# Kernel tuning notes

Measured on AMD Instinct MI355X. Metric: run time of the kernel, lower is better.

Reference implementation:

```python
import jax, jax.numpy as jnp
import numpy as np

B, S, H = 1, 4096, 2048
NH, NKV, HD = 8, 4, 256
I = 8192
EPS = 1e-6
THETA = 10000.0
WINDOW = 4096  # hardcoded sliding window for even layer_idx
LAYER_IDX = 0


def rms_norm(x, w):
    v = jnp.mean(jnp.square(x), axis=-1, keepdims=True)
    return x * jax.lax.rsqrt(v + EPS) * w


def rotate_half(x):
    h = x.shape[-1] // 2
    return jnp.concatenate([-x[..., h:], x[..., :h]], axis=-1)


def apply_rope(q, k, positions):
    # q: [B,S,NH,HD], k: [B,S,NKV,HD], positions: [B,S]
    inv_freq = 1.0 / (THETA ** (jnp.arange(0, HD, 2, dtype=jnp.float32) / HD))
    freqs = positions.astype(jnp.float32)[..., None] * inv_freq  # [B,S,HD/2]
    emb = jnp.concatenate([freqs, freqs], axis=-1)               # [B,S,HD]
    cos = jnp.cos(emb)[:, :, None, :]
    sin = jnp.sin(emb)[:, :, None, :]
    q = q * cos + rotate_half(q) * sin
    k = k * cos + rotate_half(k) * sin
    return q, k


def forward(hidden_states, q_w, k_w, v_w, o_w, gate_w, up_w, down_w, ln1_w, ln2_w,
            attention_mask, position_ids):
    # ---- input RMSNorm + attention ----
    residual = hidden_states
    x = rms_norm(hidden_states, ln1_w)

    q = (x @ q_w).reshape(B, S, NH, HD)
    k = (x @ k_w).reshape(B, S, NKV, HD)
    v = (x @ v_w).reshape(B, S, NKV, HD)
    q, k = apply_rope(q, k, position_ids)

    # GQA: repeat kv heads to match query heads
    groups = NH // NKV
    k = jnp.repeat(k, groups, axis=2)  # [B,S,NH,HD]
    v = jnp.repeat(v, groups, axis=2)

    # masks: padding mask AND causal AND (even layer) local window of WINDOW
    row = jnp.arange(S)[:, None]
    col = jnp.arange(S)[None, :]
    causal = col <= row                                   # [S,S]
    combined = causal[None, None] & (attention_mask[:, None, None, :] > 0)
    if LAYER_IDX % 2 == 0:
        keep = ~(col <= row - WINDOW)                     # mask out keys older than WINDOW
        combined = combined & keep[None, None]
    neg = jnp.finfo(jnp.float32).min
    bias = jnp.where(combined, 0.0, neg).astype(jnp.float32)  # [B,1,S,S]

    scale = HD ** -0.5
    scores = jnp.einsum('bqhd,bkhd->bhqk', q, k) * scale + bias
    probs = jax.nn.softmax(scores, axis=-1)
    attn = jnp.einsum('bhqk,bkhd->bqhd', probs, v).reshape(B, S, NH * HD)
    attn_out = attn @ o_w

    hidden_states = residual + attn_out

    # ---- post-attention RMSNorm + gated-GeLU MLP ----
    residual = hidden_states
    x = rms_norm(hidden_states, ln2_w)
    mlp = (jax.nn.gelu(x @ gate_w, approximate=True) * (x @ up_w)) @ down_w
    return residual + mlp


def setup_inputs() -> dict:
    key = jax.random.key(0)
    ks = jax.random.split(key, 9)
    std = 0.02
    n = lambda k, shp: jax.random.normal(k, shp, dtype=jnp.float32) * std
    return {
        'hidden_states': jax.random.normal(ks[0], (B, S, H), dtype=jnp.float32),
        'q_w': n(ks[1], (H, NH * HD)),
        'k_w': n(ks[2], (H, NKV * HD)),
        'v_w': n(ks[3], (H, NKV * HD)),
        'o_w': n(ks[4], (NH * HD, H)),
        'gate_w': n(ks[5], (H, I)),
        'up_w': n(ks[6], (H, I)),
        'down_w': n(ks[7], (I, H)),
        'ln1_w': jnp.ones((H,), jnp.float32),
        'ln2_w': jnp.ones((H,), jnp.float32),
        'attention_mask': jnp.ones((B, S), jnp.int32),
        'position_ids': jnp.broadcast_to(jnp.arange(S, dtype=jnp.int32)[None, :], (B, S)),
    }


def reference(hidden_states, q_w, k_w, v_w, o_w, gate_w, up_w, down_w, ln1_w, ln2_w,
              attention_mask, position_ids):
    return forward(hidden_states, q_w, k_w, v_w, o_w, gate_w, up_w, down_w,
                   ln1_w, ln2_w, attention_mask, position_ids)
```

## Files before the change

kernel.cpp:

```cpp
#include <hip/hip_runtime.h>
#include <hip/hip_bf16.h>
#include <math.h>

#define S_LEN 4096
#define HID   2048
#define NHEADS 8
#define NKVH   4
#define HDIM   256
#define FFN    8192
#define WIN    4096

typedef __bf16 bf16_t;
typedef __bf16 bf16x8 __attribute__((ext_vector_type(8)));
typedef float  floatx4 __attribute__((ext_vector_type(4)));

__device__ inline float waveReduceSum(float v) {
#pragma unroll
    for (int o = 32; o > 0; o >>= 1) v += __shfl_xor(v, o);
    return v;
}
__device__ inline float blockReduceSum(float v, float* sh) {
    int tid = threadIdx.x;
    v = waveReduceSum(v);
    if ((tid & 63) == 0) sh[tid >> 6] = v;
    __syncthreads();
    v = sh[0] + sh[1] + sh[2] + sh[3];
    __syncthreads();
    return v;
}

template <typename T>
__global__ __launch_bounds__(256) void transpose_bf16_kernel(const T* __restrict__ in,
                                                             bf16_t* __restrict__ out,
                                                             int R, int C) {
    __shared__ float tile[32][33];
    int tx = threadIdx.x & 31;
    int ty = threadIdx.x >> 5;
    int c0 = blockIdx.x * 32;
    int r0 = blockIdx.y * 32;
#pragma unroll
    for (int i = 0; i < 4; ++i)
        tile[ty + i * 8][tx] = (float)in[(long long)(r0 + ty + i * 8) * C + c0 + tx];
    __syncthreads();
#pragma unroll
    for (int i = 0; i < 4; ++i)
        out[(long long)(c0 + ty + i * 8) * R + r0 + tx] = (bf16_t)tile[tx][ty + i * 8];
}

__global__ __launch_bounds__(256) void rmsnorm_kernel(const float* __restrict__ x,
                                                      const float* __restrict__ w,
                                                      bf16_t* __restrict__ out) {
    __shared__ float sh[4];
    int row = blockIdx.x;
    const float* xr = x + (long long)row * HID;
    float v[8];
    float ss = 0.f;
#pragma unroll
    for (int i = 0; i < 8; ++i) {
        v[i] = xr[threadIdx.x + i * 256];
        ss += v[i] * v[i];
    }
    ss = blockReduceSum(ss, sh);
    float sc = rsqrtf(ss * (1.0f / HID) + 1e-6f);
#pragma unroll
    for (int i = 0; i < 8; ++i) {
        int c = threadIdx.x + i * 256;
        out[(long long)row * HID + c] = (bf16_t)(v[i] * sc * w[c]);
    }
}

__global__ __launch_bounds__(256) void rope_kernel(bf16_t* __restrict__ q,
                                                   bf16_t* __restrict__ k,
                                                   const int* __restrict__ pos_ids) {
    int s = blockIdx.x;
    float p = (float)pos_ids[s];
    for (int t = threadIdx.x; t < (NHEADS + NKVH) * (HDIM / 2); t += 256) {
        int head = t >> 7;
        int i = t & 127;
        float inv = expf(-(2.0f * (float)i / (float)HDIM) * 9.210340371976184f);
        float f = p * inv;
        float sn, cs;
        sincosf(f, &sn, &cs);
        bf16_t* base = (head < NHEADS) ? (q + (long long)s * HID + head * HDIM)
                                       : (k + (long long)s * (NKVH * HDIM) + (head - NHEADS) * HDIM);
        float a = (float)base[i];
        float b = (float)base[i + 128];
        base[i]       = (bf16_t)(a * cs - b * sn);
        base[i + 128] = (bf16_t)(b * cs + a * sn);
    }
}

__global__ __launch_bounds__(256) void flash_attn_kernel(const bf16_t* __restrict__ qg,
                                                         const bf16_t* __restrict__ kg,
                                                         const bf16_t* __restrict__ vTg,
                                                         bf16_t* __restrict__ og,
                                                         const int* __restrict__ amask) {
    __shared__ bf16_t sK[64 * 256];
    __shared__ bf16_t sV[256 * 64];

    const int h = blockIdx.y;
    const int q0 = blockIdx.x * 128;
    const int tid = threadIdx.x;
    const int lane = tid & 63;
    const int w = tid >> 6;
    const int tl = lane & 15;
    const int quad = lane >> 4;

    const bf16_t* Qh = qg + h * HDIM;
    const bf16_t* Kh = kg + (h >> 1) * HDIM;
    const bf16_t* Vh = vTg + (long long)(h >> 1) * HDIM * S_LEN;
    bf16_t* sPw = sK + w * (32 * 64);

    bf16x8 qf[2][8];
#pragma unroll
    for (int mi = 0; mi < 2; ++mi) {
        const bf16_t* qrow = Qh + (long long)(q0 + w * 32 + mi * 16 + tl) * HID;
#pragma unroll
        for (int ks = 0; ks < 8; ++ks)
            qf[mi][ks] = *(const bf16x8*)(qrow + (ks * 4 + quad) * 8);
    }

    floatx4 oacc[2][16] = {};
    float ml[2][4], ll[2][4];
#pragma unroll
    for (int mi = 0; mi < 2; ++mi)
#pragma unroll
        for (int r = 0; r < 4; ++r) { ml[mi][r] = -3e38f; ll[mi][r] = 0.f; }

    int klo = q0 - (WIN - 1);
    if (klo < 0) klo = 0;
    klo &= ~63;

    for (int kt = klo; kt < q0 + 128; kt += 64) {
#pragma unroll
        for (int it = 0; it < 8; ++it) {
            int s = it * 256 + tid;
            {
                int m = s >> 5, sg = s & 31, g = sg ^ (m & 7);
                const bf16_t* src = Kh + (long long)(kt + m) * (NKVH * HDIM) + g * 8;
                __builtin_amdgcn_global_load_lds((const __attribute__((address_space(1))) void*)src,
                                                 (__attribute__((address_space(3))) void*)(sK + s * 8),
                                                 16, 0, 0);
            }
            {
                int m = s >> 3, sg = s & 7, g = sg ^ (m & 7);
                const bf16_t* src = Vh + (long long)m * S_LEN + kt + g * 8;
                __builtin_amdgcn_global_load_lds((const __attribute__((address_space(1))) void*)src,
                                                 (__attribute__((address_space(3))) void*)(sV + s * 8),
                                                 16, 0, 0);
            }
        }
        __builtin_amdgcn_s_waitcnt(0x0f70);
        __syncthreads();

        floatx4 sacc[2][4] = {};
#pragma unroll
        for (int ks = 0; ks < 8; ++ks) {
            bf16x8 kf[4];
#pragma unroll
            for (int ni = 0; ni < 4; ++ni) {
                int row = ni * 16 + tl;
                int ph = (ks * 4 + quad) ^ (row & 7);
                kf[ni] = *(const bf16x8*)(sK + row * 256 + ph * 8);
            }
#pragma unroll
            for (int mi = 0; mi < 2; ++mi)
#pragma unroll
                for (int ni = 0; ni < 4; ++ni)
                    sacc[mi][ni] = __builtin_amdgcn_mfma_f32_16x16x32_bf16(qf[mi][ks], kf[ni], sacc[mi][ni], 0, 0, 0);
        }
        __syncthreads();

        int am[4];
#pragma unroll
        for (int ni = 0; ni < 4; ++ni) am[ni] = amask[kt + ni * 16 + tl];
#pragma unroll
        for (int mi = 0; mi < 2; ++mi) {
#pragma unroll
            for (int r = 0; r < 4; ++r) {
                int irow = q0 + w * 32 + mi * 16 + quad * 4 + r;
                float sv[4];
                float mx = -3e38f;
#pragma unroll
                for (int ni = 0; ni < 4; ++ni) {
                    int j = kt + ni * 16 + tl;
                    bool valid = (j <= irow) && (j > irow - WIN) && (am[ni] > 0);
                    float x = valid ? sacc[mi][ni][r] * 0.0625f : -3e38f;
                    sv[ni] = x;
                    mx = fmaxf(mx, x);
                }
                mx = fmaxf(mx, __shfl_xor(mx, 1));
                mx = fmaxf(mx, __shfl_xor(mx, 2));
                mx = fmaxf(mx, __shfl_xor(mx, 4));
                mx = fmaxf(mx, __shfl_xor(mx, 8));
                float mnew = fmaxf(ml[mi][r], mx);
                float alpha = __expf(ml[mi][r] - mnew);
                float rs = 0.f;
#pragma unroll
                for (int ni = 0; ni < 4; ++ni) {
                    float p = (sv[ni] > -1e37f) ? __expf(sv[ni] - mnew) : 0.f;
                    rs += p;
                    int row = mi * 16 + quad * 4 + r;
                    int col = ni * 16 + tl;
                    sPw[row * 64 + ((col >> 3) ^ (row & 7)) * 8 + (col & 7)] = (bf16_t)p;
                }
                rs += __shfl_xor(rs, 1);
                rs += __shfl_xor(rs, 2);
                rs += __shfl_xor(rs, 4);
                rs += __shfl_xor(rs, 8);
                ll[mi][r] = ll[mi][r] * alpha + rs;
                ml[mi][r] = mnew;
#pragma unroll
                for (int dt = 0; dt < 16; ++dt) oacc[mi][dt][r] *= alpha;
            }
        }

#pragma unroll
        for (int k2 = 0; k2 < 2; ++k2) {
            bf16x8 pf[2];
#pragma unroll
            for (int mi = 0; mi < 2; ++mi) {
                int row = mi * 16 + tl;
                int ph = (k2 * 4 + quad) ^ (row & 7);
                pf[mi] = *(const bf16x8*)(sPw + row * 64 + ph * 8);
            }
#pragma unroll
            for (int dt = 0; dt < 16; ++dt) {
                int d = dt * 16 + tl;
                int ph = (k2 * 4 + quad) ^ (d & 7);
                bf16x8 vf = *(const bf16x8*)(sV + d * 64 + ph * 8);
#pragma unroll
                for (int mi = 0; mi < 2; ++mi)
                    oacc[mi][dt] = __builtin_amdgcn_mfma_f32_16x16x32_bf16(pf[mi], vf, oacc[mi][dt], 0, 0, 0);
            }
        }
        __syncthreads();
    }

#pragma unroll
    for (int mi = 0; mi < 2; ++mi)
#pragma unroll
        for (int r = 0; r < 4; ++r) {
            float inv = (ll[mi][r] > 0.f) ? 1.0f / ll[mi][r] : 0.f;
            long long row = q0 + w * 32 + mi * 16 + quad * 4 + r;
#pragma unroll
            for (int dt = 0; dt < 16; ++dt)
                og[row * HID + h * HDIM + dt * 16 + tl] = (bf16_t)(oacc[mi][dt][r] * inv);
        }
}

template <int MODE>
__global__ __launch_bounds__(256) void gemm_kernel(const bf16_t* __restrict__ A, int lda,
                                                   const bf16_t* __restrict__ Bt, int ldb,
                                                   void* __restrict__ Cv, int ldc,
                                                   const void* __restrict__ aux, int K) {
    __shared__ bf16_t smem[2 * 128 * 64];
    bf16_t* sA = smem;
    bf16_t* sB = smem + 128 * 64;

    const int tid = threadIdx.x;
    const int n0 = blockIdx.x * 128;
    const int m0 = blockIdx.y * 128;

    const int lane = tid & 63;
    const int wid = tid >> 6;
    const int wm = (wid >> 1) * 64;
    const int wn = (wid & 1) * 64;
    const int tl = lane & 15;
    const int quad = lane >> 4;

    floatx4 acc[4][4] = {};

    for (int k0 = 0; k0 < K; k0 += 64) {
#pragma unroll
        for (int it = 0; it < 4; ++it) {
            int s = it * 256 + tid;
            int m = s >> 3;
            int sg = s & 7;
            int g = sg ^ (m & 7);
            const bf16_t* ga = A + (long long)(m0 + m) * lda + k0 + g * 8;
            __builtin_amdgcn_global_load_lds((const __attribute__((address_space(1))) void*)ga,
                                             (__attribute__((address_space(3))) void*)(sA + s * 8),
                                             16, 0, 0);
            const bf16_t* gb = Bt + (long long)(n0 + m) * ldb + k0 + g * 8;
            __builtin_amdgcn_global_load_lds((const __attribute__((address_space(1))) void*)gb,
                                             (__attribute__((address_space(3))) void*)(sB + s * 8),
                                             16, 0, 0);
        }
        __builtin_amdgcn_s_waitcnt(0x0f70);
        __syncthreads();

#pragma unroll
        for (int kk = 0; kk < 2; ++kk) {
            bf16x8 af[4], bfr[4];
#pragma unroll
            for (int mi = 0; mi < 4; ++mi) {
                int m = wm + mi * 16 + tl;
                int sg = (kk * 4 + quad) ^ (m & 7);
                af[mi] = *(const bf16x8*)(sA + m * 64 + sg * 8);
            }
#pragma unroll
            for (int ni = 0; ni < 4; ++ni) {
                int n = wn + ni * 16 + tl;
                int sg = (kk * 4 + quad) ^ (n & 7);
                bfr[ni] = *(const bf16x8*)(sB + n * 64 + sg * 8);
            }
#pragma unroll
            for (int mi = 0; mi < 4; ++mi)
#pragma unroll
                for (int ni = 0; ni < 4; ++ni)
                    acc[mi][ni] = __builtin_amdgcn_mfma_f32_16x16x32_bf16(af[mi], bfr[ni], acc[mi][ni], 0, 0, 0);
        }
        __syncthreads();
    }

#pragma unroll
    for (int mi = 0; mi < 4; ++mi) {
#pragma unroll
        for (int ni = 0; ni < 4; ++ni) {
#pragma unroll
            for (int r = 0; r < 4; ++r) {
                int gr = m0 + wm + mi * 16 + quad * 4 + r;
                int gc = n0 + wn + ni * 16 + tl;
                long long idx = (long long)gr * ldc + gc;
                float v = acc[mi][ni][r];
                if (MODE == 0) {
                    ((bf16_t*)Cv)[idx] = (bf16_t)v;
                } else if (MODE == 1) {
                    ((float*)Cv)[idx] = ((const float*)aux)[idx] + v;
                } else {
                    float g = (float)((const bf16_t*)aux)[idx];
                    float t = 0.7978845608028654f * (g + 0.044715f * g * g * g);
                    float ge = 0.5f * g * (1.0f + tanhf(t));
                    ((bf16_t*)Cv)[idx] = (bf16_t)(ge * v);
                }
            }
        }
    }
}

extern "C" void kernel_launch(void* const* d_in, const int* in_sizes, int n_in,
                              void* d_out, int out_size, void* d_ws, size_t ws_size,
                              hipStream_t stream) {
    const float* hidden = (const float*)d_in[0];
    const float* q_w    = (const float*)d_in[1];
    const float* k_w    = (const float*)d_in[2];
    const float* v_w    = (const float*)d_in[3];
    const float* o_w    = (const float*)d_in[4];
    const float* gate_w = (const float*)d_in[5];
    const float* up_w   = (const float*)d_in[6];
    const float* down_w = (const float*)d_in[7];
    const float* ln1_w  = (const float*)d_in[8];
    const float* ln2_w  = (const float*)d_in[9];
    const int* amask    = (const int*)d_in[10];
    const int* pos_ids  = (const int*)d_in[11];
    float* out = (float*)d_out;

    const size_t MB = 1ull << 20;
    char* ws = (char*)d_ws;
    bf16_t* wqT = (bf16_t*)(ws + 0 * MB);
    bf16_t* wkT = (bf16_t*)(ws + 8 * MB);
    bf16_t* wvT = (bf16_t*)(ws + 12 * MB);
    bf16_t* woT = (bf16_t*)(ws + 16 * MB);
    bf16_t* wgT = (bf16_t*)(ws + 24 * MB);
    bf16_t* wuT = (bf16_t*)(ws + 56 * MB);
    bf16_t* wdT = (bf16_t*)(ws + 88 * MB);
    bf16_t* xb  = (bf16_t*)(ws + 120 * MB);
    bf16_t* qb    = (bf16_t*)(ws + 136 * MB);
    bf16_t* kb    = (bf16_t*)(ws + 152 * MB);
    bf16_t* vb    = (bf16_t*)(ws + 160 * MB);
    bf16_t* vT    = (bf16_t*)(ws + 168 * MB);
    bf16_t* attnb = (bf16_t*)(ws + 176 * MB);
    bf16_t* gateb = (bf16_t*)(ws + 136 * MB);
    (void)ws_size; (void)in_sizes; (void)n_in; (void)out_size;

    dim3 blk(256);

    transpose_bf16_kernel<float><<<dim3(64, 64), blk, 0, stream>>>(q_w, wqT, 2048, 2048);
    transpose_bf16_kernel<float><<<dim3(32, 64), blk, 0, stream>>>(k_w, wkT, 2048, 1024);
    transpose_bf16_kernel<float><<<dim3(32, 64), blk, 0, stream>>>(v_w, wvT, 2048, 1024);
    transpose_bf16_kernel<float><<<dim3(64, 64), blk, 0, stream>>>(o_w, woT, 2048, 2048);
    transpose_bf16_kernel<float><<<dim3(256, 64), blk, 0, stream>>>(gate_w, wgT, 2048, 8192);
    transpose_bf16_kernel<float><<<dim3(256, 64), blk, 0, stream>>>(up_w, wuT, 2048, 8192);
    transpose_bf16_kernel<float><<<dim3(64, 256), blk, 0, stream>>>(down_w, wdT, 8192, 2048);

    rmsnorm_kernel<<<dim3(S_LEN), blk, 0, stream>>>(hidden, ln1_w, xb);

    gemm_kernel<0><<<dim3(16, 32), blk, 0, stream>>>(xb, HID, wqT, HID, qb, 2048, nullptr, HID);
    gemm_kernel<0><<<dim3(8, 32), blk, 0, stream>>>(xb, HID, wkT, HID, kb, 1024, nullptr, HID);
    gemm_kernel<0><<<dim3(8, 32), blk, 0, stream>>>(xb, HID, wvT, HID, vb, 1024, nullptr, HID);

    rope_kernel<<<dim3(S_LEN), blk, 0, stream>>>(qb, kb, pos_ids);

    transpose_bf16_kernel<bf16_t><<<dim3(32, 128), blk, 0, stream>>>(vb, vT, S_LEN, 1024);

    flash_attn_kernel<<<dim3(S_LEN / 128, NHEADS), blk, 0, stream>>>(qb, kb, vT, attnb, amask);

    gemm_kernel<1><<<dim3(16, 32), blk, 0, stream>>>(attnb, 2048, woT, 2048, out, 2048, hidden, 2048);

    rmsnorm_kernel<<<dim3(S_LEN), blk, 0, stream>>>(out, ln2_w, xb);

    gemm_kernel<0><<<dim3(64, 32), blk, 0, stream>>>(xb, HID, wgT, HID, gateb, FFN, nullptr, HID);
    gemm_kernel<2><<<dim3(64, 32), blk, 0, stream>>>(xb, HID, wuT, HID, gateb, FFN, gateb, HID);
    gemm_kernel<1><<<dim3(16, 32), blk, 0, stream>>>(gateb, FFN, wdT, FFN, out, 2048, out, FFN);
}
```

Before: 1.404 ms.

## Split attention KV range across blocks with causal load balancing and combine pass

Rewrites flash attention to use 64-row query tiles. Each block processes a mirrored pair of query tiles (i and 63-i) so causal work is balanced. The KV range is split in two across blockIdx.z, with partial outputs and (max, sum) stats written out and merged by a new combine kernel. It also transposes the score MFMA so softmax reductions run across quads, and it vectorises the mask loads and P stores. The aim is more parallelism and better load balance, at the cost of extra partial-output traffic and an additional kernel launch.

Result: faster. 1.304 ms (-7.1%).

```diff
diff --git a/kernel.cpp b/kernel.cpp
--- a/kernel.cpp
+++ b/kernel.cpp
@@ -11,6 +11,7 @@
 #define WIN    4096
 
 typedef __bf16 bf16_t;
+typedef __bf16 bf16x4 __attribute__((ext_vector_type(4)));
 typedef __bf16 bf16x8 __attribute__((ext_vector_type(8)));
 typedef float  floatx4 __attribute__((ext_vector_type(4)));
 
@@ -93,13 +94,15 @@
 __global__ __launch_bounds__(256) void flash_attn_kernel(const bf16_t* __restrict__ qg,
                                                          const bf16_t* __restrict__ kg,
                                                          const bf16_t* __restrict__ vTg,
-                                                         bf16_t* __restrict__ og,
+                                                         bf16_t* __restrict__ op0,
+                                                         bf16_t* __restrict__ op1,
+                                                         float* __restrict__ mlb,
                                                          const int* __restrict__ amask) {
     __shared__ bf16_t sK[64 * 256];
     __shared__ bf16_t sV[256 * 64];
 
     const int h = blockIdx.y;
-    const int q0 = blockIdx.x * 128;
+    const int kh = blockIdx.z;
     const int tid = threadIdx.x;
     const int lane = tid & 63;
     const int w = tid >> 6;
@@ -109,144 +112,162 @@
     const bf16_t* Qh = qg + h * HDIM;
     const bf16_t* Kh = kg + (h >> 1) * HDIM;
     const bf16_t* Vh = vTg + (long long)(h >> 1) * HDIM * S_LEN;
-    bf16_t* sPw = sK + w * (32 * 64);
-
-    bf16x8 qf[2][8];
-#pragma unroll
-    for (int mi = 0; mi < 2; ++mi) {
-        const bf16_t* qrow = Qh + (long long)(q0 + w * 32 + mi * 16 + tl) * HID;
+    bf16_t* Op = kh ? op1 : op0;
+    bf16_t* sP = sK + w * (16 * 72);
+
+#pragma unroll 1
+    for (int half = 0; half < 2; ++half) {
+        const int qi = half ? (63 - blockIdx.x) : blockIdx.x;
+        const int qr0 = qi * 64;
+        const int ntiles = qi + 1;
+        const int mid = ntiles >> 1;
+        const int t0 = kh ? mid : 0;
+        const int t1 = kh ? ntiles : mid;
+        const int irow = qr0 + w * 16 + tl;
+
+        const bf16_t* qrow = Qh + (long long)irow * HID;
+        bf16x8 qf[8];
 #pragma unroll
         for (int ks = 0; ks < 8; ++ks)
-            qf[mi][ks] = *(const bf16x8*)(qrow + (ks * 4 + quad) * 8);
-    }
-
-    floatx4 oacc[2][16] = {};
-    float ml[2][4], ll[2][4];
-#pragma unroll
-    for (int mi = 0; mi < 2; ++mi)
-#pragma unroll
-        for (int r = 0; r < 4; ++r) { ml[mi][r] = -3e38f; ll[mi][r] = 0.f; }
-
-    int klo = q0 - (WIN - 1);
-    if (klo < 0) klo = 0;
-    klo &= ~63;
-
-    for (int kt = klo; kt < q0 + 128; kt += 64) {
-#pragma unroll
-        for (int it = 0; it < 8; ++it) {
-            int s = it * 256 + tid;
-            {
-                int m = s >> 5, sg = s & 31, g = sg ^ (m & 7);
-                const bf16_t* src = Kh + (long long)(kt + m) * (NKVH * HDIM) + g * 8;
-                __builtin_amdgcn_global_load_lds((const __attribute__((address_space(1))) void*)src,
-                                                 (__attribute__((address_space(3))) void*)(sK + s * 8),
-                                                 16, 0, 0);
-            }
-            {
-                int m = s >> 3, sg = s & 7, g = sg ^ (m & 7);
-                const bf16_t* src = Vh + (long long)m * S_LEN + kt + g * 8;
-                __builtin_amdgcn_global_load_lds((const __attribute__((address_space(1))) void*)src,
-                                                 (__attribute__((address_space(3))) void*)(sV + s * 8),
-                                                 16, 0, 0);
-            }
-        }
-        __builtin_amdgcn_s_waitcnt(0x0f70);
-        __syncthreads();
-
-        floatx4 sacc[2][4] = {};
-#pragma unroll
-        for (int ks = 0; ks < 8; ++ks) {
-            bf16x8 kf[4];
+            qf[ks] = *(const bf16x8*)(qrow + (ks * 4 + quad) * 8);
+
+        floatx4 oacc[16] = {};
+        float m_i = -3e38f, l_i = 0.f;
+
+        for (int t = t0; t < t1; ++t) {
+            const int kt = t * 64;
+#pragma unroll
+            for (int it = 0; it < 8; ++it) {
+                int s = it * 256 + tid;
+                {
+                    int m = s >> 5, sg = s & 31, g = sg ^ (m & 7);
+                    const bf16_t* src = Kh + (long long)(kt + m) * (NKVH * HDIM) + g * 8;
+                    __builtin_amdgcn_global_load_lds((const __attribute__((address_space(1))) void*)src,
+                                                     (__attribute__((address_space(3))) void*)(sK + s * 8),
+                                                     16, 0, 0);
+                }
+                {
+                    int m = s >> 3, sg = s & 7, g = sg ^ (m & 7);
+                    const bf16_t* src = Vh + (long long)m * S_LEN + kt + g * 8;
+                    __builtin_amdgcn_global_load_lds((const __attribute__((address_space(1))) void*)src,
+                                                     (__attribute__((address_space(3))) void*)(sV + s * 8),
+                                                     16, 0, 0);
+                }
+            }
+            __builtin_amdgcn_s_waitcnt(0x0f70);
+            __syncthreads();
+
+            floatx4 sacc[4] = {};
+#pragma unroll
+            for (int ks = 0; ks < 8; ++ks) {
+                bf16x8 kf[4];
+#pragma unroll
+                for (int ni = 0; ni < 4; ++ni) {
+                    int row = ni * 16 + tl;
+                    int ph = (ks * 4 + quad) ^ (row & 7);
+                    kf[ni] = *(const bf16x8*)(sK + row * 256 + ph * 8);
+                }
+#pragma unroll
+                for (int ni = 0; ni < 4; ++ni)
+                    sacc[ni] = __builtin_amdgcn_mfma_f32_16x16x32_bf16(kf[ni], qf[ks], sacc[ni], 0, 0, 0);
+            }
+            __syncthreads();
+
+            float sv[4][4];
+            float mx = -3e38f;
 #pragma unroll
             for (int ni = 0; ni < 4; ++ni) {
-                int row = ni * 16 + tl;
-                int ph = (ks * 4 + quad) ^ (row & 7);
-                kf[ni] = *(const bf16x8*)(sK + row * 256 + ph * 8);
-            }
-#pragma unroll
-            for (int mi = 0; mi < 2; ++mi)
-#pragma unroll
-                for (int ni = 0; ni < 4; ++ni)
-                    sacc[mi][ni] = __builtin_amdgcn_mfma_f32_16x16x32_bf16(qf[mi][ks], kf[ni], sacc[mi][ni], 0, 0, 0);
-        }
-        __syncthreads();
-
-        int am[4];
-#pragma unroll
-        for (int ni = 0; ni < 4; ++ni) am[ni] = amask[kt + ni * 16 + tl];
-#pragma unroll
-        for (int mi = 0; mi < 2; ++mi) {
+                int4 am = *(const int4*)(amask + kt + ni * 16 + quad * 4);
+#pragma unroll
+                for (int r = 0; r < 4; ++r) {
+                    int j = kt + ni * 16 + quad * 4 + r;
+                    int amr = (r == 0) ? am.x : (r == 1) ? am.y : (r == 2) ? am.z : am.w;
+                    bool valid = (j <= irow) && (j > irow - WIN) && (amr > 0);
+                    float x = valid ? sacc[ni][r] * 0.0625f : -3e38f;
+                    sv[ni][r] = x;
+                    mx = fmaxf(mx, x);
+                }
+            }
+            mx = fmaxf(mx, __shfl_xor(mx, 16));
+            mx = fmaxf(mx, __shfl_xor(mx, 32));
+            float mnew = fmaxf(m_i, mx);
+            float alpha = __expf(m_i - mnew);
+            float rs = 0.f;
+#pragma unroll
+            for (int ni = 0; ni < 4; ++ni) {
+                bf16x4 pk;
+#pragma unroll
+                for (int r = 0; r < 4; ++r) {
+                    float p = (sv[ni][r] > -1e37f) ? __expf(sv[ni][r] - mnew) : 0.f;
+                    rs += p;
+                    pk[r] = (bf16_t)p;
+                }
+                *(bf16x4*)(sP + tl * 72 + ni * 16 + quad * 4) = pk;
+            }
+            rs += __shfl_xor(rs, 16);
+            rs += __shfl_xor(rs, 32);
+            l_i = l_i * alpha + rs;
+            m_i = mnew;
+
+            floatx4 av;
+#pragma unroll
+            for (int r = 0; r < 4; ++r) av[r] = __shfl(alpha, quad * 4 + r);
+#pragma unroll
+            for (int dt = 0; dt < 16; ++dt) oacc[dt] *= av;
+
+#pragma unroll
+            for (int k2 = 0; k2 < 2; ++k2) {
+                bf16x8 pf = *(const bf16x8*)(sP + tl * 72 + k2 * 32 + quad * 8);
+#pragma unroll
+                for (int dt = 0; dt < 16; ++dt) {
+                    int d = dt * 16 + tl;
+                    int ph = (k2 * 4 + quad) ^ (d & 7);
+                    bf16x8 vf = *(const bf16x8*)(sV + d * 64 + ph * 8);
+                    oacc[dt] = __builtin_amdgcn_mfma_f32_16x16x32_bf16(pf, vf, oacc[dt], 0, 0, 0);
+                }
+            }
+            __syncthreads();
+        }
+
+        floatx4 inv;
+#pragma unroll
+        for (int r = 0; r < 4; ++r) {
+            float lv = __shfl(l_i, quad * 4 + r);
+            inv[r] = (lv > 0.f) ? 1.0f / lv : 0.f;
+        }
+#pragma unroll
+        for (int dt = 0; dt < 16; ++dt) {
 #pragma unroll
             for (int r = 0; r < 4; ++r) {
-                int irow = q0 + w * 32 + mi * 16 + quad * 4 + r;
-                float sv[4];
-                float mx = -3e38f;
-#pragma unroll
-                for (int ni = 0; ni < 4; ++ni) {
-                    int j = kt + ni * 16 + tl;
-                    bool valid = (j <= irow) && (j > irow - WIN) && (am[ni] > 0);
-                    float x = valid ? sacc[mi][ni][r] * 0.0625f : -3e38f;
-                    sv[ni] = x;
-                    mx = fmaxf(mx, x);
-                }
-                mx = fmaxf(mx, __shfl_xor(mx, 1));
-                mx = fmaxf(mx, __shfl_xor(mx, 2));
-                mx = fmaxf(mx, __shfl_xor(mx, 4));
-                mx = fmaxf(mx, __shfl_xor(mx, 8));
-                float mnew = fmaxf(ml[mi][r], mx);
-                float alpha = __expf(ml[mi][r] - mnew);
-                float rs = 0.f;
-#pragma unroll
-                for (int ni = 0; ni < 4; ++ni) {
-                    float p = (sv[ni] > -1e37f) ? __expf(sv[ni] - mnew) : 0.f;
-                    rs += p;
-                    int row = mi * 16 + quad * 4 + r;
-                    int col = ni * 16 + tl;
-                    sPw[row * 64 + ((col >> 3) ^ (row & 7)) * 8 + (col & 7)] = (bf16_t)p;
-                }
-                rs += __shfl_xor(rs, 1);
-                rs += __shfl_xor(rs, 2);
-                rs += __shfl_xor(rs, 4);
-                rs += __shfl_xor(rs, 8);
-                ll[mi][r] = ll[mi][r] * alpha + rs;
-                ml[mi][r] = mnew;
-#pragma unroll
-                for (int dt = 0; dt < 16; ++dt) oacc[mi][dt][r] *= alpha;
-            }
-        }
-
-#pragma unroll
-        for (int k2 = 0; k2 < 2; ++k2) {
-            bf16x8 pf[2];
-#pragma unroll
-            for (int mi = 0; mi < 2; ++mi) {
-                int row = mi * 16 + tl;
-                int ph = (k2 * 4 + quad) ^ (row & 7);
-                pf[mi] = *(const bf16x8*)(sPw + row * 64 + ph * 8);
-            }
-#pragma unroll
-            for (int dt = 0; dt < 16; ++dt) {
-                int d = dt * 16 + tl;
-                int ph = (k2 * 4 + quad) ^ (d & 7);
-                bf16x8 vf = *(const bf16x8*)(sV + d * 64 + ph * 8);
-#pragma unroll
-                for (int mi = 0; mi < 2; ++mi)
-                    oacc[mi][dt] = __builtin_amdgcn_mfma_f32_16x16x32_bf16(pf[mi], vf, oacc[mi][dt], 0, 0, 0);
-            }
-        }
-        __syncthreads();
-    }
-
-#pragma unroll
-    for (int mi = 0; mi < 2; ++mi)
-#pragma unroll
-        for (int r = 0; r < 4; ++r) {
-            float inv = (ll[mi][r] > 0.f) ? 1.0f / ll[mi][r] : 0.f;
-            long long row = q0 + w * 32 + mi * 16 + quad * 4 + r;
-#pragma unroll
-            for (int dt = 0; dt < 16; ++dt)
-                og[row * HID + h * HDIM + dt * 16 + tl] = (bf16_t)(oacc[mi][dt][r] * inv);
-        }
+                long long row = qr0 + w * 16 + quad * 4 + r;
+                Op[row * HID + h * HDIM + dt * 16 + tl] = (bf16_t)(oacc[dt][r] * inv[r]);
+            }
+        }
+        if (quad == 0) {
+            long long mi = ((long long)(kh * NHEADS + h) * S_LEN + qr0 + w * 16 + tl) * 2;
+            mlb[mi] = m_i;
+            mlb[mi + 1] = l_i;
+        }
+    }
+}
+
+__global__ __launch_bounds__(256) void combine_kernel(bf16_t* __restrict__ op0,
+                                                      const bf16_t* __restrict__ op1,
+                                                      const float* __restrict__ mlb) {
+    int h = blockIdx.x;
+    int row = blockIdx.y;
+    int d = threadIdx.x;
+    long long m0i = ((long long)h * S_LEN + row) * 2;
+    long long m1i = ((long long)(NHEADS + h) * S_LEN + row) * 2;
+    float m0 = mlb[m0i], l0 = mlb[m0i + 1];
+    float m1 = mlb[m1i], l1 = mlb[m1i + 1];
+    float M = fmaxf(m0, m1);
+    float w0 = (l0 > 0.f) ? l0 * __expf(m0 - M) : 0.f;
+    float w1 = (l1 > 0.f) ? l1 * __expf(m1 - M) : 0.f;
+    float inv = 1.0f / (w0 + w1);
+    long long idx = (long long)row * HID + h * HDIM + d;
+    float v = (w0 * (float)op0[idx] + w1 * (float)op1[idx]) * inv;
+    op0[idx] = (bf16_t)v;
 }
 
 template <int MODE>
@@ -365,12 +386,16 @@
     bf16_t* wgT = (bf16_t*)(ws + 24 * MB);
     bf16_t* wuT = (bf16_t*)(ws + 56 * MB);
     bf16_t* wdT = (bf16_t*)(ws + 88 * MB);
-    bf16_t* xb  = (bf16_t*)(ws + 120 * MB);
+    bf16_t* xb    = (bf16_t*)(ws + 120 * MB);
     bf16_t* qb    = (bf16_t*)(ws + 136 * MB);
     bf16_t* kb    = (bf16_t*)(ws + 152 * MB);
     bf16_t* vb    = (bf16_t*)(ws + 160 * MB);
     bf16_t* vT    = (bf16_t*)(ws + 168 * MB);
-    bf16_t* attnb = (bf16_t*)(ws + 176 * MB);
+    bf16_t* op0   = (bf16_t*)(ws + 120 * MB);
+    bf16_t* op1   = (bf16_t*)(ws + 176 * MB);
+    float*  mlb   = (float*) (ws + 192 * MB);
+    bf16_t* attnb = (bf16_t*)(ws + 120 * MB);
+    bf16_t* xb2   = (bf16_t*)(ws + 120 * MB);
     bf16_t* gateb = (bf16_t*)(ws + 136 * MB);
     (void)ws_size; (void)in_sizes; (void)n_in; (void)out_size;
 
@@ -394,13 +419,14 @@
 
     transpose_bf16_kernel<bf16_t><<<dim3(32, 128), blk, 0, stream>>>(vb, vT, S_LEN, 1024);
 
-    flash_attn_kernel<<<dim3(S_LEN / 128, NHEADS), blk, 0, stream>>>(qb, kb, vT, attnb, amask);
+    flash_attn_kernel<<<dim3(32, NHEADS, 2), blk, 0, stream>>>(qb, kb, vT, op0, op1, mlb, amask);
+    combine_kernel<<<dim3(NHEADS, S_LEN), blk, 0, stream>>>(op0, op1, mlb);
 
     gemm_kernel<1><<<dim3(16, 32), blk, 0, stream>>>(attnb, 2048, woT, 2048, out, 2048, hidden, 2048);
 
-    rmsnorm_kernel<<<dim3(S_LEN), blk, 0, stream>>>(out, ln2_w, xb);
-
-    gemm_kernel<0><<<dim3(64, 32), blk, 0, stream>>>(xb, HID, wgT, HID, gateb, FFN, nullptr, HID);
-    gemm_kernel<2><<<dim3(64, 32), blk, 0, stream>>>(xb, HID, wuT, HID, gateb, FFN, gateb, HID);
+    rmsnorm_kernel<<<dim3(S_LEN), blk, 0, stream>>>(out, ln2_w, xb2);
+
+    gemm_kernel<0><<<dim3(64, 32), blk, 0, stream>>>(xb2, HID, wgT, HID, gateb, FFN, nullptr, HID);
+    gemm_kernel<2><<<dim3(64, 32), blk, 0, stream>>>(xb2, HID, wuT, HID, gateb, FFN, gateb, HID);
     gemm_kernel<1><<<dim3(16, 32), blk, 0, stream>>>(gateb, FFN, wdT, FFN, out, 2048, out, FFN);
 }
```
